# Kernel tuning notes

Hardware: AMD Instinct MI355X
Metric: run time of the kernel (lower is better)

The kernel has to match this reference:

```python
import jax, jax.numpy as jnp
import numpy as np

N = 10000   # nodes per graph copy
E = 50000   # directed edges before to_undirected
B = 4       # batch size (graph is repeated B times)
K = 16      # num_neg + 1
D = 64      # in_dim == out_dim
R = 200     # num_relation (embedding table has 2R rows)
L = 3       # num_layer
NODE_RATIO = 0.1
DEGREE_RATIO = 1.0


def setup_inputs() -> dict:
    key = jax.random.key(0)
    ks = jax.random.split(key, 16)
    s = 0.05
    edge_index = jax.random.randint(ks[0], (2, E), 0, N, dtype=jnp.int32)
    edge_attr = jax.random.randint(ks[1], (E,), 0, R, dtype=jnp.int32)
    # asserts in source require h and r constant along the negative axis
    h_index = jnp.tile(jax.random.randint(ks[2], (B, 1), 0, N, dtype=jnp.int32), (1, K))
    r_index = jnp.tile(jax.random.randint(ks[3], (B, 1), 0, R, dtype=jnp.int32), (1, K))
    t_index = jax.random.randint(ks[4], (B, K), 0, N, dtype=jnp.int32)
    return {
        'h_index': h_index, 'r_index': r_index, 't_index': t_index,
        'hidden_states': jax.random.normal(ks[5], (B, D), jnp.float32),
        'rel_hidden_states': jax.random.normal(ks[6], (2 * R, D), jnp.float32),
        'edge_index': edge_index, 'edge_attr': edge_attr,
        'score_text_embs': jax.random.normal(ks[7], (N, D), jnp.float32) * 0.1,
        'all_index': jnp.arange(N, dtype=jnp.int32),
        'rel_emb_table': jax.random.normal(ks[8], (2 * R, D), jnp.float32) * s,
        'W_lin': jax.random.normal(ks[9], (2 * D, D), jnp.float32) * s,
        'b_lin': jnp.zeros((D,), jnp.float32),
        'W_mlp1': jax.random.normal(ks[10], (D, 2 * D), jnp.float32) * s,
        'b_mlp1': jnp.zeros((2 * D,), jnp.float32),
        'W_mlp2': jax.random.normal(ks[11], (2 * D, 1), jnp.float32) * s,
        'b_mlp2': jnp.zeros((1,), jnp.float32),
        'rel_w': 1.0 + jax.random.normal(ks[12], (L, 2 * R, D), jnp.float32) * s,
        'conv_W': jax.random.normal(ks[13], (L, 12 * D, D), jnp.float32) * s,
        'conv_b': jnp.zeros((L, D), jnp.float32),
    }


def _score(hidden, rel, W_lin, b_lin, W1, b1, W2, b2):
    # linear(cat[hidden, rel]) -> heuristic; mlp(hidden * heuristic) -> scalar
    heur = jnp.concatenate([hidden, rel], axis=-1) @ W_lin + b_lin
    x = hidden * heur
    h = jax.nn.relu(x @ W1 + b1)
    return (h @ W2 + b2)[..., 0]


def _forward(h_index, r_index, t_index, hidden_states, rel_hidden_states,
             edge_index, edge_attr, score_text_embs, all_index, rel_emb_table,
             W_lin, b_lin, W_mlp1, b_mlp1, W_mlp2, b_mlp2, rel_w, conv_W, conv_b):
    f32 = hidden_states.dtype
    # --- to_undirected: add reversed edges (edge_attr copied, as in PyG) ---
    ei = jnp.concatenate([edge_index, edge_index[::-1]], axis=1)      # [2, 2E]
    ea = jnp.concatenate([edge_attr, edge_attr])                       # [2E]
    E2 = 2 * E
    # --- _repeat_graph: B copies with node-index offsets ---
    offsets = jnp.arange(B, dtype=jnp.int32) * N
    ei_b = jnp.transpose(ei[None] + offsets[:, None, None], (1, 0, 2)).reshape(2, B * E2)
    ea_b = jnp.tile(ea, B)
    Nt, Et = B * N, B * E2
    src, dst = ei_b[0], ei_b[1]
    h0 = h_index[:, 0] + offsets                                       # [B]
    t_full = t_index + offsets[:, None]                                # [B, K]
    rel_embeds = rel_emb_table[r_index[:, 0]].astype(f32)              # [B, D]
    # --- init_input_embeds: tail text embeds then head embeds; score at heads ---
    input_embeds = jnp.zeros((Nt, D), f32).at[all_index].set(score_text_embs)
    input_embeds = input_embeds.at[h0].set(hidden_states)
    score = jnp.zeros((Nt,), f32).at[h0].set(
        _score(hidden_states, rel_embeds, W_lin, b_lin, W_mlp1, b_mlp1, W_mlp2, b_mlp2))
    query0 = rel_embeds[0]   # index_batch is all-zeros in source -> query[0] everywhere
    # --- pna degree mean over the full batched graph ---
    deg_in_full = jax.ops.segment_sum(jnp.ones((Et,), f32), dst, num_segments=Nt)
    pna_mean = jnp.mean(jnp.log(deg_in_full + 1.0))
    ks_n = max(1, int(NODE_RATIO * Nt))
    es = max(1, int(DEGREE_RATIO * ks_n * Et / Nt))
    hidden = input_embeds
    for l in range(L):
        # select_edges: top-ks nodes by score, then top-es outgoing edges
        thr = jax.lax.top_k(score, ks_n)[0][-1]
        s_src = score[src]
        edge_score = jnp.where(s_src >= thr, s_src, -jnp.inf)
        thr_e = jax.lax.top_k(edge_score, es)[0][-1]
        emask = (edge_score >= thr_e) & jnp.isfinite(edge_score)       # [Et]
        em = emask.astype(f32)
        # relation-conditioned messages gated by sigmoid(score of source)
        m = jax.nn.sigmoid(s_src)[:, None] * hidden[src] * rel_w[l][ea_b]
        mf = m * em[:, None]
        deg = jax.ops.segment_sum(em, dst, num_segments=Nt)            # [Nt]
        denom = jnp.maximum(deg, 1.0)[:, None]
        mean_a = jax.ops.segment_sum(mf, dst, num_segments=Nt) / denom
        sq = jax.ops.segment_sum(mf * mf, dst, num_segments=Nt) / denom
        std = jnp.sqrt(jnp.maximum(sq - mean_a * mean_a, 0.0) + 1e-6)
        mmax = jax.ops.segment_max(jnp.where(emask[:, None], m, -jnp.inf), dst, num_segments=Nt)
        mmin = jax.ops.segment_min(jnp.where(emask[:, None], m, jnp.inf), dst, num_segments=Nt)
        has = (deg > 0)[:, None]
        mmax = jnp.where(has, mmax, 0.0)
        mmin = jnp.where(has, mmin, 0.0)
        feat = jnp.concatenate([mean_a, mmax, mmin, std], axis=-1)     # [Nt, 4D]
        sc_log = jnp.log(deg + 1.0)
        amp = (sc_log / pna_mean)[:, None]
        att = (pna_mean / (sc_log + 1e-6))[:, None]
        feat_all = jnp.concatenate([feat, feat * amp, feat * att], -1)  # [Nt, 12D]
        upd = jax.nn.relu(feat_all @ conv_W[l] + conv_b[l])            # [Nt, D]
        out_deg = jax.ops.segment_sum(em, src, num_segments=Nt)
        omask = out_deg > 0
        hidden = jnp.where(omask[:, None], hidden + upd, hidden)
        new_score = _score(hidden, jnp.broadcast_to(query0, hidden.shape),
                           W_lin, b_lin, W_mlp1, b_mlp1, W_mlp2, b_mlp2)
        score = jnp.where(omask, new_score, score)
    return score[t_full]                                               # [B, K]


def reference(h_index, r_index, t_index, hidden_states, rel_hidden_states,
              edge_index, edge_attr, score_text_embs, all_index, rel_emb_table,
              W_lin, b_lin, W_mlp1, b_mlp1, W_mlp2, b_mlp2, rel_w, conv_W, conv_b):
    return _forward(h_index, r_index, t_index, hidden_states, rel_hidden_states,
                    edge_index, edge_attr, score_text_embs, all_index, rel_emb_table,
                    W_lin, b_lin, W_mlp1, b_mlp1, W_mlp2, b_mlp2, rel_w, conv_W, conv_b)
```

## Files before the change

kernel.cpp:

```cpp
#include <hip/hip_runtime.h>
#include <math.h>

#define N_NODES 10000
#define E_EDGES 50000
#define NT      40000
#define KS_N    4000
#define ES_E    40000
#define WTOT    400000u
#define CHUNK   16384

__device__ __forceinline__ unsigned f2u(float f) {
    unsigned b = __float_as_uint(f);
    return (b & 0x80000000u) ? ~b : (b | 0x80000000u);
}
__device__ __forceinline__ float u2f(unsigned u) {
    unsigned b = (u & 0x80000000u) ? (u & 0x7fffffffu) : ~u;
    return __uint_as_float(b);
}
__device__ __forceinline__ float wave_sum64(float x) {
    for (int off = 32; off > 0; off >>= 1) x += __shfl_down(x, off, 64);
    return x;
}

__global__ void count_deg(const int* __restrict__ ei, unsigned* __restrict__ deg) {
    int j = blockIdx.x * 256 + threadIdx.x;
    if (j < E_EDGES) {
        atomicAdd(&deg[ei[j]], 1u);
        atomicAdd(&deg[ei[E_EDGES + j]], 1u);
    }
}

__global__ __launch_bounds__(1024) void scan_degrees(const unsigned* __restrict__ deg,
                                                     unsigned* __restrict__ rowptr,
                                                     unsigned* __restrict__ cursor) {
    __shared__ unsigned wsum[16];
    __shared__ unsigned carry;
    int tid = threadIdx.x, lane = tid & 63, w = tid >> 6;
    if (tid == 0) carry = 0;
    __syncthreads();
    for (int base = 0; base < N_NODES; base += 1024) {
        int i = base + tid;
        unsigned v = (i < N_NODES) ? deg[i] : 0u;
        unsigned x = v;
        for (int off = 1; off < 64; off <<= 1) {
            unsigned y = __shfl_up(x, off, 64);
            if (lane >= off) x += y;
        }
        if (lane == 63) wsum[w] = x;
        __syncthreads();
        if (tid < 16) {
            unsigned s = wsum[tid];
            for (int off = 1; off < 16; off <<= 1) {
                unsigned y = __shfl_up(s, off, 64);
                if (tid >= off) s += y;
            }
            wsum[tid] = s;
        }
        __syncthreads();
        unsigned woff = (w > 0) ? wsum[w - 1] : 0u;
        unsigned excl = carry + woff + x - v;
        if (i < N_NODES) { rowptr[i] = excl; cursor[i] = excl; }
        __syncthreads();
        if (tid == 0) carry += wsum[15];
        __syncthreads();
    }
    if (tid == 0) rowptr[N_NODES] = carry;
}

__global__ void scatter_edges(const int* __restrict__ ei, const int* __restrict__ ea,
                              unsigned* __restrict__ cursor, unsigned* __restrict__ inedge) {
    int j = blockIdx.x * 256 + threadIdx.x;
    if (j < E_EDGES) {
        unsigned s = (unsigned)ei[j];
        unsigned d = (unsigned)ei[E_EDGES + j];
        unsigned a = (unsigned)ea[j];
        unsigned p1 = atomicAdd(&cursor[d], 1u);
        inedge[p1] = s | (a << 16);
        unsigned p2 = atomicAdd(&cursor[s], 1u);
        inedge[p2] = d | (a << 16);
    }
}

__global__ void tile_degb(const unsigned* __restrict__ degb, unsigned* __restrict__ degbt) {
    int v = blockIdx.x * 256 + threadIdx.x;
    if (v < NT) degbt[v] = degb[v % N_NODES];
}

__global__ __launch_bounds__(1024) void pna_kernel(const unsigned* __restrict__ degb,
                                                   float* __restrict__ scalars) {
    __shared__ float ws[16];
    int tid = threadIdx.x;
    float s = 0.0f;
    for (int i = tid; i < N_NODES; i += 1024) s += logf((float)degb[i] + 1.0f);
    for (int off = 32; off > 0; off >>= 1) s += __shfl_down(s, off, 64);
    if ((tid & 63) == 0) ws[tid >> 6] = s;
    __syncthreads();
    if (tid == 0) {
        float t = 0.0f;
        for (int i = 0; i < 16; ++i) t += ws[i];
        scalars[3] = t / (float)N_NODES;
    }
}

__global__ void init_hidden(const float* __restrict__ text, float* __restrict__ hidden) {
    int i = blockIdx.x * 256 + threadIdx.x;
    if (i < NT * 64) {
        int v = i >> 6;
        hidden[i] = (v < N_NODES) ? text[i] : 0.0f;
    }
}

__device__ float wave_score_g(float hid, float rel, const float* Wlin, const float* blin,
                              const float* W1, const float* b1, const float* W2, float b2v,
                              int lane) {
    float heur = blin[lane];
    for (int i = 0; i < 64; ++i) heur += __shfl(hid, i, 64) * Wlin[i * 64 + lane];
    for (int i = 0; i < 64; ++i) heur += __shfl(rel, i, 64) * Wlin[(64 + i) * 64 + lane];
    float x = hid * heur;
    float a0 = b1[lane], a1 = b1[64 + lane];
    for (int i = 0; i < 64; ++i) {
        float xv = __shfl(x, i, 64);
        a0 += xv * W1[i * 128 + lane];
        a1 += xv * W1[i * 128 + 64 + lane];
    }
    a0 = fmaxf(a0, 0.0f); a1 = fmaxf(a1, 0.0f);
    float part = a0 * W2[lane] + a1 * W2[64 + lane];
    part = wave_sum64(part);
    part = __shfl(part, 0, 64);
    return part + b2v;
}

__global__ void init_heads(const int* __restrict__ h_index, const int* __restrict__ r_index,
                           const float* __restrict__ hidden_states,
                           const float* __restrict__ rel_table,
                           const float* __restrict__ W_lin, const float* __restrict__ b_lin,
                           const float* __restrict__ W1, const float* __restrict__ b1,
                           const float* __restrict__ W2, const float* __restrict__ b2,
                           float* __restrict__ hidden, float* __restrict__ score,
                           float* __restrict__ qh) {
    __shared__ float q0[64];
    int tid = threadIdx.x, w = tid >> 6, lane = tid & 63;
    int b = w;
    int h0 = h_index[b * 16] + b * N_NODES;
    float hs  = hidden_states[b * 64 + lane];
    float rel = rel_table[r_index[b * 16] * 64 + lane];
    hidden[h0 * 64 + lane] = hs;
    if (b == 0) q0[lane] = rel;
    float s = wave_score_g(hs, rel, W_lin, b_lin, W1, b1, W2, b2[0], lane);
    if (lane == 0) score[h0] = s;
    __syncthreads();
    if (w == 0) {
        float acc = b_lin[lane];
        for (int i = 0; i < 64; ++i) acc += q0[i] * W_lin[(64 + i) * 64 + lane];
        qh[lane] = acc;
    }
}

__device__ void block_pick(unsigned h, unsigned r, unsigned* outd, unsigned* outr,
                           unsigned* scr) {
    int tid = threadIdx.x, lane = tid & 63, w = tid >> 6;
    __syncthreads();
    unsigned x = h;
    for (int off = 1; off < 64; off <<= 1) {
        unsigned y = __shfl_up(x, off, 64);
        if (lane >= off) x += y;
    }
    if (lane == 63) scr[w] = x;
    __syncthreads();
    unsigned woff = 0;
    for (int i = 0; i < 4; ++i) if (i < w) woff += scr[i];
    unsigned excl = woff + x - h;
    if (r >= excl && r < excl + h) { scr[4] = (unsigned)tid; scr[5] = r - excl; }
    __syncthreads();
    *outd = scr[4]; *outr = scr[5];
}

__global__ __launch_bounds__(256) void select_pass(
    const float* __restrict__ score, const unsigned* __restrict__ degbt,
    unsigned* __restrict__ ghn, unsigned* __restrict__ ghw,
    unsigned* __restrict__ state, float* __restrict__ scalars,
    unsigned* __restrict__ countp, int pass) {
    __shared__ unsigned lh[512];
    __shared__ unsigned scr[8];
    __shared__ unsigned sh_last;
    int tid = threadIdx.x;
    lh[tid] = 0; lh[256 + tid] = 0;
    __syncthreads();
    unsigned pn = state[0], pw = state[2];
    int shift = 24 - pass * 8;
    for (int v = blockIdx.x * 256 + tid; v < NT; v += gridDim.x * 256) {
        unsigned key = f2u(score[v]);
        unsigned wg = degbt[v];
        unsigned dig = (key >> shift) & 255u;
        if (pass == 0) {
            atomicAdd(&lh[dig], 1u);
            if (wg) atomicAdd(&lh[256 + dig], wg);
        } else {
            unsigned hi = key >> (shift + 8);
            if (hi == pn) atomicAdd(&lh[dig], 1u);
            if (wg && hi == pw) atomicAdd(&lh[256 + dig], wg);
        }
    }
    __syncthreads();
    if (lh[tid]) atomicAdd(&ghn[tid], lh[tid]);
    if (lh[256 + tid]) atomicAdd(&ghw[tid], lh[256 + tid]);
    __threadfence();
    if (tid == 0) sh_last = atomicAdd(&state[8 + pass], 1u);
    __syncthreads();
    if (sh_last != gridDim.x - 1) return;
    unsigned hn = atomicAdd(&ghn[tid], 0u);
    unsigned hw = atomicAdd(&ghw[tid], 0u);
    ghn[tid] = 0; ghw[tid] = 0;
    unsigned rn, rw_;
    if (pass == 0) { pn = 0; rn = NT - KS_N; pw = 0; rw_ = WTOT - ES_E; }
    else { rn = state[1]; rw_ = state[3]; }
    unsigned dn, rn2, dw, rw2;
    block_pick(hn, rn, &dn, &rn2, scr);
    block_pick(hw, rw_, &dw, &rw2, scr);
    if (tid == 0) {
        pn = (pn << 8) | dn;
        pw = (pw << 8) | dw;
        state[0] = pn; state[1] = rn2; state[2] = pw; state[3] = rw2;
        state[8 + pass] = 0;
        if (pass == 3) {
            float thr = u2f(pn), thre = u2f(pw);
            scalars[0] = thr;
            scalars[1] = fmaxf(thr, thre);
            *countp = 0;
        }
    }
}

__global__ void compact_sig(const float* __restrict__ score, const unsigned* __restrict__ degbt,
                            const float* __restrict__ scalars, unsigned* __restrict__ countp,
                            int* __restrict__ list, float* __restrict__ sigp) {
    int v = blockIdx.x * 256 + threadIdx.x;
    if (v >= NT) return;
    float sc = score[v];
    bool pass = sc >= scalars[1];
    float sg = -1.0f;
    if (pass) sg = 1.0f / (1.0f + expf(-sc));
    sigp[v] = sg;
    if (pass && degbt[v] > 0) {
        unsigned p = atomicAdd(countp, 1u);
        list[p] = v;
    }
}

__global__ __launch_bounds__(256) void agg_feat(
    const float* __restrict__ sigp, const float* __restrict__ hidden,
    const unsigned* __restrict__ rowptr, const unsigned* __restrict__ inedge,
    const float* __restrict__ rel_w, const float* __restrict__ scalars,
    const unsigned* __restrict__ countp, const int* __restrict__ list,
    float* __restrict__ feat, float* __restrict__ ampatt, int layer,
    int mbase, int climit) {
    int count = (int)*countp;
    int cc = count - mbase; if (cc > climit) cc = climit;
    int tid = threadIdx.x, w = tid >> 6, lane = tid & 63;
    int li = blockIdx.x * 4 + w;
    if (li >= cc) return;
    int v = list[mbase + li];
    int b = v / N_NODES;
    int boff = b * N_NODES;
    int n = v - boff;
    const float* rw = rel_w + (size_t)layer * 400 * 64;
    unsigned r0 = rowptr[n], r1 = rowptr[n + 1];
    float sum = 0.f, sq = 0.f, mx = -INFINITY, mn = INFINITY;
    int cnt = 0;
    #pragma unroll 2
    for (unsigned e = r0; e < r1; ++e) {
        unsigned pk = inedge[e];
        int src = (int)(pk & 0xffffu) + boff;
        float sg = sigp[src];
        float h  = hidden[((size_t)src << 6) + lane];
        float rv = rw[((size_t)(pk >> 16) << 6) + lane];
        bool valid = sg >= 0.0f;
        float mval = sg * h * rv;
        if (valid) { sum += mval; sq += mval * mval; }
        mx = fmaxf(mx, valid ? mval : -INFINITY);
        mn = fminf(mn, valid ? mval : INFINITY);
        cnt += valid ? 1 : 0;
    }
    float denom = cnt > 0 ? (float)cnt : 1.0f;
    float mean = sum / denom;
    float sd = sqrtf(fmaxf(sq / denom - mean * mean, 0.0f) + 1e-6f);
    float* fr = feat + ((size_t)li << 8);
    fr[lane]        = mean;
    fr[64 + lane]   = cnt > 0 ? mx : 0.0f;
    fr[128 + lane]  = cnt > 0 ? mn : 0.0f;
    fr[192 + lane]  = sd;
    if (lane == 0) {
        float pna = scalars[3];
        float sl = logf((float)cnt + 1.0f);
        ampatt[li * 2]     = sl / pna;
        ampatt[li * 2 + 1] = pna / (sl + 1e-6f);
    }
}

#define FMA4(C, av, bv) { C[0] += av * bv.x; C[1] += av * bv.y; C[2] += av * bv.z; C[3] += av * bv.w; }

__global__ __launch_bounds__(256) void gemm_upd(
    const float* __restrict__ conv_W, const float* __restrict__ conv_b,
    const unsigned* __restrict__ countp, const float* __restrict__ feat,
    const float* __restrict__ ampatt, float* __restrict__ updc,
    int layer, int mbase, int climit) {
    __shared__ float sA[32][34];
    __shared__ float sB[32][196];
    __shared__ float sAmp[32], sAtt[32];
    int count = (int)*countp;
    int cc = count - mbase; if (cc > climit) cc = climit;
    int m0 = blockIdx.x * 32;
    if (m0 >= cc) return;
    int tid = threadIdx.x;
    if (tid < 32) {
        int rl = m0 + tid;
        float a = 0.f, t = 0.f;
        if (rl < cc) { a = ampatt[rl * 2]; t = ampatt[rl * 2 + 1]; }
        sAmp[tid] = a; sAtt[tid] = t;
    }
    int mg = tid >> 4, ng = tid & 15;
    int j0 = ng * 4;
    float c0[2][4] = {}, c1[2][4] = {}, c2[2][4] = {};
    const float* Wl = conv_W + (size_t)layer * 768 * 64;
    const float4* feat4 = (const float4*)feat;
    int arow = tid >> 3, akq = tid & 7;
    for (int k0 = 0; k0 < 256; k0 += 32) {
        __syncthreads();
        {
            float4 va = feat4[(((size_t)(m0 + arow)) << 6) + (k0 >> 2) + akq];
            sA[akq * 4 + 0][arow] = va.x; sA[akq * 4 + 1][arow] = va.y;
            sA[akq * 4 + 2][arow] = va.z; sA[akq * 4 + 3][arow] = va.w;
        }
        #pragma unroll
        for (int it = 0; it < 6; ++it) {
            int fi = it * 256 + tid;
            int rr = fi >> 4, q = fi & 15;
            int part = rr >> 5, kk = rr & 31;
            float4 vb = *(const float4*)(Wl + (((size_t)(part * 256 + k0 + kk)) << 6) + q * 4);
            float* d = &sB[kk][part * 64 + q * 4];
            d[0] = vb.x; d[1] = vb.y; d[2] = vb.z; d[3] = vb.w;
        }
        __syncthreads();
        #pragma unroll 4
        for (int kk = 0; kk < 32; ++kk) {
            float a0 = sA[kk][mg * 2];
            float a1 = sA[kk][mg * 2 + 1];
            float4 b0 = *(const float4*)&sB[kk][j0];
            float4 b1 = *(const float4*)&sB[kk][64 + j0];
            float4 b2 = *(const float4*)&sB[kk][128 + j0];
            FMA4(c0[0], a0, b0) FMA4(c0[1], a1, b0)
            FMA4(c1[0], a0, b1) FMA4(c1[1], a1, b1)
            FMA4(c2[0], a0, b2) FMA4(c2[1], a1, b2)
        }
    }
    const float4 bias = *(const float4*)(conv_b + layer * 64 + j0);
    #pragma unroll
    for (int mi = 0; mi < 2; ++mi) {
        int ml = mg * 2 + mi;
        int rl = m0 + ml;
        if (rl < cc) {
            float amp = sAmp[ml], att = sAtt[ml];
            float4 o;
            o.x = fmaxf(c0[mi][0] + amp * c1[mi][0] + att * c2[mi][0] + bias.x, 0.0f);
            o.y = fmaxf(c0[mi][1] + amp * c1[mi][1] + att * c2[mi][1] + bias.y, 0.0f);
            o.z = fmaxf(c0[mi][2] + amp * c1[mi][2] + att * c2[mi][2] + bias.z, 0.0f);
            o.w = fmaxf(c0[mi][3] + amp * c1[mi][3] + att * c2[mi][3] + bias.w, 0.0f);
            *(float4*)(updc + (((size_t)(mbase + rl)) << 6) + j0) = o;
        }
    }
}

__global__ __launch_bounds__(256) void apply_score_gemm(
    float* __restrict__ hidden, const float* __restrict__ updc,
    float* __restrict__ score, const unsigned* __restrict__ countp,
    const int* __restrict__ list,
    const float* __restrict__ W_lin, const float* __restrict__ qh,
    const float* __restrict__ W1, const float* __restrict__ b1,
    const float* __restrict__ W2, const float* __restrict__ b2) {
    __shared__ float sH[64][65];
    __shared__ float sX[64][65];
    int count = (int)*countp;
    int m0 = blockIdx.x * 64;
    if (m0 >= count) return;
    int tid = threadIdx.x;

    {
        int q = tid & 15;
        int mB = tid >> 4;
        #pragma unroll
        for (int r = 0; r < 4; ++r) {
            int m = r * 16 + mB;
            int idx = m0 + m;
            float4 hv = {0.f, 0.f, 0.f, 0.f};
            if (idx < count) {
                int v = list[idx];
                hv = *(const float4*)&hidden[((size_t)v << 6) + q * 4];
                float4 uv = *(const float4*)&updc[((size_t)idx << 6) + q * 4];
                hv.x += uv.x; hv.y += uv.y; hv.z += uv.z; hv.w += uv.w;
                *(float4*)&hidden[((size_t)v << 6) + q * 4] = hv;
            }
            sH[m][q * 4 + 0] = hv.x; sH[m][q * 4 + 1] = hv.y;
            sH[m][q * 4 + 2] = hv.z; sH[m][q * 4 + 3] = hv.w;
        }
    }
    __syncthreads();

    int mg = tid >> 4, ng = tid & 15;
    const float4* Wl4 = (const float4*)W_lin;
    const float4* W14 = (const float4*)W1;
    const float4* qh4 = (const float4*)qh;
    const float4* b14 = (const float4*)b1;
    const float4* W24 = (const float4*)W2;

    {
        float4 qv = qh4[ng];
        float acc[4][4];
        #pragma unroll
        for (int mi = 0; mi < 4; ++mi) {
            acc[mi][0] = qv.x; acc[mi][1] = qv.y; acc[mi][2] = qv.z; acc[mi][3] = qv.w;
        }
        for (int k = 0; k < 64; ++k) {
            float4 bv = Wl4[k * 16 + ng];
            #pragma unroll
            for (int mi = 0; mi < 4; ++mi) {
                float av = sH[mg * 4 + mi][k];
                acc[mi][0] += av * bv.x; acc[mi][1] += av * bv.y;
                acc[mi][2] += av * bv.z; acc[mi][3] += av * bv.w;
            }
        }
        #pragma unroll
        for (int mi = 0; mi < 4; ++mi) {
            int m = mg * 4 + mi;
            #pragma unroll
            for (int ni = 0; ni < 4; ++ni)
                sX[m][ng * 4 + ni] = sH[m][ng * 4 + ni] * acc[mi][ni];
        }
    }
    __syncthreads();

    {
        float4 bA = b14[ng], bB = b14[16 + ng];
        float accA[4][4], accB[4][4];
        #pragma unroll
        for (int mi = 0; mi < 4; ++mi) {
            accA[mi][0] = bA.x; accA[mi][1] = bA.y; accA[mi][2] = bA.z; accA[mi][3] = bA.w;
            accB[mi][0] = bB.x; accB[mi][1] = bB.y; accB[mi][2] = bB.z; accB[mi][3] = bB.w;
        }
        for (int k = 0; k < 64; ++k) {
            float4 bvA = W14[k * 32 + ng];
            float4 bvB = W14[k * 32 + 16 + ng];
            #pragma unroll
            for (int mi = 0; mi < 4; ++mi) {
                float av = sX[mg * 4 + mi][k];
                accA[mi][0] += av * bvA.x; accA[mi][1] += av * bvA.y;
                accA[mi][2] += av * bvA.z; accA[mi][3] += av * bvA.w;
                accB[mi][0] += av * bvB.x; accB[mi][1] += av * bvB.y;
                accB[mi][2] += av * bvB.z; accB[mi][3] += av * bvB.w;
            }
        }
        float4 w2A = W24[ng], w2B = W24[16 + ng];
        #pragma unroll
        for (int mi = 0; mi < 4; ++mi) {
            int m = mg * 4 + mi;
            float pA0 = fmaxf(accA[mi][0], 0.f), pB0 = fmaxf(accB[mi][0], 0.f);
            float pA1 = fmaxf(accA[mi][1], 0.f), pB1 = fmaxf(accB[mi][1], 0.f);
            float pA2 = fmaxf(accA[mi][2], 0.f), pB2 = fmaxf(accB[mi][2], 0.f);
            float pA3 = fmaxf(accA[mi][3], 0.f), pB3 = fmaxf(accB[mi][3], 0.f);
            sH[m][ng * 4 + 0] = pA0 * w2A.x + pB0 * w2B.x;
            sH[m][ng * 4 + 1] = pA1 * w2A.y + pB1 * w2B.y;
            sH[m][ng * 4 + 2] = pA2 * w2A.z + pB2 * w2B.z;
            sH[m][ng * 4 + 3] = pA3 * w2A.w + pB3 * w2B.w;
        }
    }
    __syncthreads();

    {
        float b2v = b2[0];
        int w = tid >> 6, lane = tid & 63;
        #pragma unroll 4
        for (int t = 0; t < 16; ++t) {
            int m = w * 16 + t;
            float p = sH[m][lane];
            float s = wave_sum64(p);
            if (lane == 0) {
                int idx = m0 + m;
                if (idx < count) score[list[idx]] = s + b2v;
            }
        }
    }
}

__global__ void gather_out(const float* __restrict__ score, const int* __restrict__ t_index,
                           float* __restrict__ out) {
    int i = threadIdx.x;
    int b = i >> 4;
    out[i] = score[t_index[i] + b * N_NODES];
}

extern "C" void kernel_launch(void* const* d_in, const int* in_sizes, int n_in,
                              void* d_out, int out_size, void* d_ws, size_t ws_size,
                              hipStream_t stream) {
    const int*   h_index       = (const int*)d_in[0];
    const int*   r_index       = (const int*)d_in[1];
    const int*   t_index       = (const int*)d_in[2];
    const float* hidden_states = (const float*)d_in[3];
    const int*   edge_index    = (const int*)d_in[5];
    const int*   edge_attr     = (const int*)d_in[6];
    const float* text          = (const float*)d_in[7];
    const float* rel_table     = (const float*)d_in[9];
    const float* W_lin         = (const float*)d_in[10];
    const float* b_lin         = (const float*)d_in[11];
    const float* W1            = (const float*)d_in[12];
    const float* b1            = (const float*)d_in[13];
    const float* W2            = (const float*)d_in[14];
    const float* b2            = (const float*)d_in[15];
    const float* rel_w         = (const float*)d_in[16];
    const float* conv_W        = (const float*)d_in[17];
    const float* conv_b        = (const float*)d_in[18];

    auto layout_bytes = [](size_t fch) -> size_t {
        auto al = [](size_t x) { return (x + 255) & ~(size_t)255; };
        size_t o = 0;
        o += al(256) * 3;
        o += al(1024) * 2;
        o += al((size_t)NT * 4);
        o += al((size_t)N_NODES * 4);
        o += al(256);
        o += al((size_t)NT * 4);
        o += al((size_t)NT * 64 * 4);
        o += al((size_t)NT * 64 * 4);
        o += al(fch * 256 * 4);
        o += al(fch * 2 * 4);
        o += al((size_t)NT * 4);
        o += al((size_t)NT * 4);
        o += al((size_t)(N_NODES + 1) * 4);
        o += al((size_t)N_NODES * 4);
        o += al((size_t)2 * E_EDGES * 4);
        return o;
    };
    const size_t FCH = (layout_bytes(NT) <= ws_size) ? (size_t)NT : (size_t)CHUNK;
    const int NCH = (FCH == (size_t)NT) ? 1 : 3;

    char* ws = (char*)d_ws;
    size_t off = 0;
    auto carve = [&](size_t bytes) -> char* {
        char* p = ws + off;
        off = (off + bytes + 255) & ~(size_t)255;
        return p;
    };
    float*    scalars = (float*)carve(256);
    unsigned* state   = (unsigned*)carve(256);
    unsigned* countp  = (unsigned*)carve(256);
    unsigned* ghn     = (unsigned*)carve(1024);
    unsigned* ghw     = (unsigned*)carve(1024);
    float*    score   = (float*)carve((size_t)NT * 4);
    unsigned* degb    = (unsigned*)carve((size_t)N_NODES * 4);
    size_t zero_end = off;
    float*    qh      = (float*)carve(256);
    float*    sigp    = (float*)carve((size_t)NT * 4);
    float*    hidden  = (float*)carve((size_t)NT * 64 * 4);
    float*    updc    = (float*)carve((size_t)NT * 64 * 4);
    float*    feat    = (float*)carve(FCH * 256 * 4);
    float*    ampatt  = (float*)carve(FCH * 2 * 4);
    int*      list    = (int*)carve((size_t)NT * 4);
    unsigned* degbt   = (unsigned*)carve((size_t)NT * 4);
    unsigned* rowptr  = (unsigned*)carve((size_t)(N_NODES + 1) * 4);
    unsigned* cursor  = (unsigned*)carve((size_t)N_NODES * 4);
    unsigned* inedge  = (unsigned*)carve((size_t)2 * E_EDGES * 4);
    if (off > ws_size) return;

    hipMemsetAsync(ws, 0, zero_end, stream);

    count_deg<<<(E_EDGES + 255) / 256, 256, 0, stream>>>(edge_index, degb);
    scan_degrees<<<1, 1024, 0, stream>>>(degb, rowptr, cursor);
    scatter_edges<<<(E_EDGES + 255) / 256, 256, 0, stream>>>(edge_index, edge_attr, cursor, inedge);
    tile_degb<<<(NT + 255) / 256, 256, 0, stream>>>(degb, degbt);
    pna_kernel<<<1, 1024, 0, stream>>>(degb, scalars);
    init_hidden<<<(NT * 64 + 255) / 256, 256, 0, stream>>>(text, hidden);
    init_heads<<<1, 256, 0, stream>>>(h_index, r_index, hidden_states, rel_table,
                                      W_lin, b_lin, W1, b1, W2, b2, hidden, score, qh);

    const int climit  = (int)FCH;
    const int aggGrid = climit / 4;
    const int gemGrid = climit / 32;
    for (int l = 0; l < 3; ++l) {
        for (int p = 0; p < 4; ++p)
            select_pass<<<40, 256, 0, stream>>>(score, degbt, ghn, ghw, state,
                                                scalars, countp, p);
        compact_sig<<<(NT + 255) / 256, 256, 0, stream>>>(score, degbt, scalars,
                                                          countp, list, sigp);
        for (int c = 0; c < NCH; ++c) {
            int mbase = c * climit;
            agg_feat<<<aggGrid, 256, 0, stream>>>(sigp, hidden, rowptr, inedge, rel_w,
                                                  scalars, countp, list, feat, ampatt,
                                                  l, mbase, climit);
            gemm_upd<<<gemGrid, 256, 0, stream>>>(conv_W, conv_b, countp, feat, ampatt,
                                                  updc, l, mbase, climit);
        }
        apply_score_gemm<<<(NT + 63) / 64, 256, 0, stream>>>(hidden, updc, score, countp,
                                                             list, W_lin, qh, W1, b1, W2, b2);
    }
    gather_out<<<1, 64, 0, stream>>>(score, t_index, (float*)d_out);
}
```

Baseline: 437.2 us.

## Fuse radix-select passes and compaction into one persistent kernel; widen GEMM tile

The four select_pass launches and compact_sig are merged into one 40-block kernel that uses a global spin barrier (state[9] epoch counter) between radix passes, which cuts five launches per layer down to one. The tiled degree array is dropped in favour of indexing degb with v % N, which removes the tile_degb kernel. Separately, gemm_upd goes from 32-row to 64-row tiles with 4x4 micro-tiles per thread to get more reuse of the B tile. The spin barrier depends on all 40 blocks being resident at the same time, and the larger tile halves the GEMM grid.

```diff
diff --git a/kernel.cpp b/kernel.cpp
--- a/kernel.cpp
+++ b/kernel.cpp
@@ -8,6 +8,7 @@
 #define ES_E    40000
 #define WTOT    400000u
 #define CHUNK   16384
+#define SEL_BLOCKS 40
 
 __device__ __forceinline__ unsigned f2u(float f) {
     unsigned b = __float_as_uint(f);
@@ -79,11 +80,6 @@
         unsigned p2 = atomicAdd(&cursor[s], 1u);
         inedge[p2] = d | (a << 16);
     }
-}
-
-__global__ void tile_degb(const unsigned* __restrict__ degb, unsigned* __restrict__ degbt) {
-    int v = blockIdx.x * 256 + threadIdx.x;
-    if (v < NT) degbt[v] = degb[v % N_NODES];
 }
 
 __global__ __launch_bounds__(1024) void pna_kernel(const unsigned* __restrict__ degb,
@@ -175,75 +171,89 @@
     *outd = scr[4]; *outr = scr[5];
 }
 
-__global__ __launch_bounds__(256) void select_pass(
-    const float* __restrict__ score, const unsigned* __restrict__ degbt,
+__global__ __launch_bounds__(256) void select_compact(
+    const float* __restrict__ score, const unsigned* __restrict__ degb,
     unsigned* __restrict__ ghn, unsigned* __restrict__ ghw,
     unsigned* __restrict__ state, float* __restrict__ scalars,
-    unsigned* __restrict__ countp, int pass) {
+    unsigned* __restrict__ countp, int* __restrict__ list,
+    float* __restrict__ sigp, int rbase) {
     __shared__ unsigned lh[512];
     __shared__ unsigned scr[8];
-    __shared__ unsigned sh_last;
+    __shared__ unsigned sh_flag;
+    __shared__ unsigned sh_state[4];
     int tid = threadIdx.x;
-    lh[tid] = 0; lh[256 + tid] = 0;
-    __syncthreads();
-    unsigned pn = state[0], pw = state[2];
-    int shift = 24 - pass * 8;
-    for (int v = blockIdx.x * 256 + tid; v < NT; v += gridDim.x * 256) {
-        unsigned key = f2u(score[v]);
-        unsigned wg = degbt[v];
-        unsigned dig = (key >> shift) & 255u;
-        if (pass == 0) {
-            atomicAdd(&lh[dig], 1u);
-            if (wg) atomicAdd(&lh[256 + dig], wg);
-        } else {
-            unsigned hi = key >> (shift + 8);
-            if (hi == pn) atomicAdd(&lh[dig], 1u);
-            if (wg && hi == pw) atomicAdd(&lh[256 + dig], wg);
-        }
-    }
-    __syncthreads();
-    if (lh[tid]) atomicAdd(&ghn[tid], lh[tid]);
-    if (lh[256 + tid]) atomicAdd(&ghw[tid], lh[256 + tid]);
-    __threadfence();
-    if (tid == 0) sh_last = atomicAdd(&state[8 + pass], 1u);
-    __syncthreads();
-    if (sh_last != gridDim.x - 1) return;
-    unsigned hn = atomicAdd(&ghn[tid], 0u);
-    unsigned hw = atomicAdd(&ghw[tid], 0u);
-    ghn[tid] = 0; ghw[tid] = 0;
-    unsigned rn, rw_;
-    if (pass == 0) { pn = 0; rn = NT - KS_N; pw = 0; rw_ = WTOT - ES_E; }
-    else { rn = state[1]; rw_ = state[3]; }
-    unsigned dn, rn2, dw, rw2;
-    block_pick(hn, rn, &dn, &rn2, scr);
-    block_pick(hw, rw_, &dw, &rw2, scr);
-    if (tid == 0) {
-        pn = (pn << 8) | dn;
-        pw = (pw << 8) | dw;
-        state[0] = pn; state[1] = rn2; state[2] = pw; state[3] = rw2;
-        state[8 + pass] = 0;
-        if (pass == 3) {
-            float thr = u2f(pn), thre = u2f(pw);
-            scalars[0] = thr;
-            scalars[1] = fmaxf(thr, thre);
-            *countp = 0;
-        }
-    }
-}
-
-__global__ void compact_sig(const float* __restrict__ score, const unsigned* __restrict__ degbt,
-                            const float* __restrict__ scalars, unsigned* __restrict__ countp,
-                            int* __restrict__ list, float* __restrict__ sigp) {
-    int v = blockIdx.x * 256 + threadIdx.x;
-    if (v >= NT) return;
-    float sc = score[v];
-    bool pass = sc >= scalars[1];
-    float sg = -1.0f;
-    if (pass) sg = 1.0f / (1.0f + expf(-sc));
-    sigp[v] = sg;
-    if (pass && degbt[v] > 0) {
-        unsigned p = atomicAdd(countp, 1u);
-        list[p] = v;
+    unsigned pn = 0, pw = 0;
+    unsigned rn = NT - KS_N, rw_ = WTOT - ES_E;
+    for (int pass = 0; pass < 4; ++pass) {
+        lh[tid] = 0; lh[256 + tid] = 0;
+        __syncthreads();
+        int shift = 24 - pass * 8;
+        for (int v = blockIdx.x * 256 + tid; v < NT; v += SEL_BLOCKS * 256) {
+            unsigned key = f2u(score[v]);
+            unsigned wg = degb[v % N_NODES];
+            unsigned dig = (key >> shift) & 255u;
+            if (pass == 0) {
+                atomicAdd(&lh[dig], 1u);
+                if (wg) atomicAdd(&lh[256 + dig], wg);
+            } else {
+                unsigned hi = key >> (shift + 8);
+                if (hi == pn) atomicAdd(&lh[dig], 1u);
+                if (wg && hi == pw) atomicAdd(&lh[256 + dig], wg);
+            }
+        }
+        __syncthreads();
+        if (lh[tid]) atomicAdd(&ghn[tid], lh[tid]);
+        if (lh[256 + tid]) atomicAdd(&ghw[tid], lh[256 + tid]);
+        __threadfence();
+        __syncthreads();
+        if (tid == 0)
+            sh_flag = (atomicAdd(&state[8], 1u) == SEL_BLOCKS - 1) ? 1u : 0u;
+        __syncthreads();
+        unsigned tgt = (unsigned)(rbase + pass + 1);
+        if (sh_flag) {
+            unsigned hn = atomicAdd(&ghn[tid], 0u);
+            unsigned hw = atomicAdd(&ghw[tid], 0u);
+            ghn[tid] = 0; ghw[tid] = 0;
+            unsigned dn, rn2, dw, rw2;
+            block_pick(hn, rn, &dn, &rn2, scr);
+            block_pick(hw, rw_, &dw, &rw2, scr);
+            if (tid == 0) {
+                pn = (pn << 8) | dn;
+                pw = (pw << 8) | dw;
+                state[0] = pn; state[1] = rn2; state[2] = pw; state[3] = rw2;
+                state[8] = 0;
+                if (pass == 3) {
+                    float thr = u2f(pn), thre = u2f(pw);
+                    scalars[0] = thr;
+                    scalars[1] = fmaxf(thr, thre);
+                    *countp = 0;
+                }
+                __threadfence();
+                atomicExch(&state[9], tgt);
+            }
+        }
+        if (tid == 0) {
+            while (atomicAdd(&state[9], 0u) < tgt) __builtin_amdgcn_s_sleep(8);
+            sh_state[0] = atomicAdd(&state[0], 0u);
+            sh_state[1] = atomicAdd(&state[1], 0u);
+            sh_state[2] = atomicAdd(&state[2], 0u);
+            sh_state[3] = atomicAdd(&state[3], 0u);
+        }
+        __syncthreads();
+        pn = sh_state[0]; rn = sh_state[1]; pw = sh_state[2]; rw_ = sh_state[3];
+    }
+    float thr = u2f(pn);
+    float THR = fmaxf(thr, u2f(pw));
+    for (int v = blockIdx.x * 256 + tid; v < NT; v += SEL_BLOCKS * 256) {
+        float sc = score[v];
+        bool ok = sc >= THR;
+        float sg = -1.0f;
+        if (ok) sg = 1.0f / (1.0f + expf(-sc));
+        sigp[v] = sg;
+        if (ok && degb[v % N_NODES] > 0) {
+            unsigned p = atomicAdd(countp, 1u);
+            list[p] = v;
+        }
     }
 }
 
@@ -304,15 +314,15 @@
     const unsigned* __restrict__ countp, const float* __restrict__ feat,
     const float* __restrict__ ampatt, float* __restrict__ updc,
     int layer, int mbase, int climit) {
-    __shared__ float sA[32][34];
+    __shared__ float sA[32][68];
     __shared__ float sB[32][196];
-    __shared__ float sAmp[32], sAtt[32];
+    __shared__ float sAmp[64], sAtt[64];
     int count = (int)*countp;
     int cc = count - mbase; if (cc > climit) cc = climit;
-    int m0 = blockIdx.x * 32;
+    int m0 = blockIdx.x * 64;
     if (m0 >= cc) return;
     int tid = threadIdx.x;
-    if (tid < 32) {
+    if (tid < 64) {
         int rl = m0 + tid;
         float a = 0.f, t = 0.f;
         if (rl < cc) { a = ampatt[rl * 2]; t = ampatt[rl * 2 + 1]; }
@@ -320,13 +330,15 @@
     }
     int mg = tid >> 4, ng = tid & 15;
     int j0 = ng * 4;
-    float c0[2][4] = {}, c1[2][4] = {}, c2[2][4] = {};
+    float c0[4][4] = {}, c1[4][4] = {}, c2[4][4] = {};
     const float* Wl = conv_W + (size_t)layer * 768 * 64;
     const float4* feat4 = (const float4*)feat;
-    int arow = tid >> 3, akq = tid & 7;
     for (int k0 = 0; k0 < 256; k0 += 32) {
         __syncthreads();
-        {
+        #pragma unroll
+        for (int it = 0; it < 2; ++it) {
+            int fi = it * 256 + tid;
+            int arow = fi >> 3, akq = fi & 7;
             float4 va = feat4[(((size_t)(m0 + arow)) << 6) + (k0 >> 2) + akq];
             sA[akq * 4 + 0][arow] = va.x; sA[akq * 4 + 1][arow] = va.y;
             sA[akq * 4 + 2][arow] = va.z; sA[akq * 4 + 3][arow] = va.w;
@@ -343,20 +355,19 @@
         __syncthreads();
         #pragma unroll 4
         for (int kk = 0; kk < 32; ++kk) {
-            float a0 = sA[kk][mg * 2];
-            float a1 = sA[kk][mg * 2 + 1];
+            float4 a  = *(const float4*)&sA[kk][mg * 4];
             float4 b0 = *(const float4*)&sB[kk][j0];
             float4 b1 = *(const float4*)&sB[kk][64 + j0];
             float4 b2 = *(const float4*)&sB[kk][128 + j0];
-            FMA4(c0[0], a0, b0) FMA4(c0[1], a1, b0)
-            FMA4(c1[0], a0, b1) FMA4(c1[1], a1, b1)
-            FMA4(c2[0], a0, b2) FMA4(c2[1], a1, b2)
+            FMA4(c0[0], a.x, b0) FMA4(c0[1], a.y, b0) FMA4(c0[2], a.z, b0) FMA4(c0[3], a.w, b0)
+            FMA4(c1[0], a.x, b1) FMA4(c1[1], a.y, b1) FMA4(c1[2], a.z, b1) FMA4(c1[3], a.w, b1)
+            FMA4(c2[0], a.x, b2) FMA4(c2[1], a.y, b2) FMA4(c2[2], a.z, b2) FMA4(c2[3], a.w, b2)
         }
     }
     const float4 bias = *(const float4*)(conv_b + layer * 64 + j0);
     #pragma unroll
-    for (int mi = 0; mi < 2; ++mi) {
-        int ml = mg * 2 + mi;
+    for (int mi = 0; mi < 4; ++mi) {
+        int ml = mg * 4 + mi;
         int rl = m0 + ml;
         if (rl < cc) {
             float amp = sAmp[ml], att = sAtt[ml];
@@ -531,7 +542,6 @@
         o += al((size_t)NT * 64 * 4);
         o += al(fch * 256 * 4);
         o += al(fch * 2 * 4);
-        o += al((size_t)NT * 4);
         o += al((size_t)NT * 4);
         o += al((size_t)(N_NODES + 1) * 4);
         o += al((size_t)N_NODES * 4);
@@ -563,7 +573,6 @@
     float*    feat    = (float*)carve(FCH * 256 * 4);
     float*    ampatt  = (float*)carve(FCH * 2 * 4);
     int*      list    = (int*)carve((size_t)NT * 4);
-    unsigned* degbt   = (unsigned*)carve((size_t)NT * 4);
     unsigned* rowptr  = (unsigned*)carve((size_t)(N_NODES + 1) * 4);
     unsigned* cursor  = (unsigned*)carve((size_t)N_NODES * 4);
     unsigned* inedge  = (unsigned*)carve((size_t)2 * E_EDGES * 4);
@@ -574,7 +583,6 @@
     count_deg<<<(E_EDGES + 255) / 256, 256, 0, stream>>>(edge_index, degb);
     scan_degrees<<<1, 1024, 0, stream>>>(degb, rowptr, cursor);
     scatter_edges<<<(E_EDGES + 255) / 256, 256, 0, stream>>>(edge_index, edge_attr, cursor, inedge);
-    tile_degb<<<(NT + 255) / 256, 256, 0, stream>>>(degb, degbt);
     pna_kernel<<<1, 1024, 0, stream>>>(degb, scalars);
     init_hidden<<<(NT * 64 + 255) / 256, 256, 0, stream>>>(text, hidden);
     init_heads<<<1, 256, 0, stream>>>(h_index, r_index, hidden_states, rel_table,
@@ -582,13 +590,10 @@
 
     const int climit  = (int)FCH;
     const int aggGrid = climit / 4;
-    const int gemGrid = climit / 32;
+    const int gemGrid = climit / 64;
     for (int l = 0; l < 3; ++l) {
-        for (int p = 0; p < 4; ++p)
-            select_pass<<<40, 256, 0, stream>>>(score, degbt, ghn, ghw, state,
-                                                scalars, countp, p);
-        compact_sig<<<(NT + 255) / 256, 256, 0, stream>>>(score, degbt, scalars,
-                                                          countp, list, sigp);
+        select_compact<<<SEL_BLOCKS, 256, 0, stream>>>(score, degb, ghn, ghw, state,
+                                                       scalars, countp, list, sigp, l * 4);
         for (int c = 0; c < NCH; ++c) {
             int mbase = c * climit;
             agg_feat<<<aggGrid, 256, 0, stream>>>(sigp, hidden, rowptr, inedge, rel_w,
```

Result: slower. 466.5 us (+6.7%).
